# Performance work log

Hardware: AMD Instinct MI355X
Metric: run time of the kernel (lower is better)

The kernel has to match this reference:

```python
import jax, jax.numpy as jnp
import numpy as np


def _maxpool2x2(t):
    # t: [B, C, H, W] -> [B, C, H//2, W//2]
    B, C, H, W = t.shape
    return t.reshape(B, C, H // 2, 2, W // 2, 2).max(axis=(3, 5))


def setup_inputs() -> dict:
    key = jax.random.key(0)
    ks = jax.random.split(key, 6)
    ch = 64
    B, H, W = 16, 64, 64
    x = jax.random.normal(ks[0], (B, ch, H, W), dtype=jnp.float32)
    # 1x1 conv weights (spectral-norm wrapper just rescales weights; use unit-scale weights)
    w_theta = jax.random.normal(ks[1], (ch // 8, ch), dtype=jnp.float32) * 0.05
    w_phi = jax.random.normal(ks[2], (ch // 8, ch), dtype=jnp.float32) * 0.05
    w_g = jax.random.normal(ks[3], (ch // 2, ch), dtype=jnp.float32) * 0.05
    w_o = jax.random.normal(ks[4], (ch, ch // 2), dtype=jnp.float32) * 0.05
    gamma = jnp.float32(0.5)  # nonzero so attention branch contributes
    return {"x": x, "w_theta": w_theta, "w_phi": w_phi, "w_g": w_g, "w_o": w_o, "gamma": gamma}


def reference(x, w_theta, w_phi, w_g, w_o, gamma):
    B, C, H, W = x.shape
    N = H * W
    # 1x1 convs are channel contractions
    theta = jnp.einsum('oc,bchw->bohw', w_theta, x).reshape(B, -1, N)          # [B, C/8, N]
    phi = _maxpool2x2(jnp.einsum('oc,bchw->bohw', w_phi, x)).reshape(B, -1, N // 4)  # [B, C/8, N/4]
    g = _maxpool2x2(jnp.einsum('oc,bchw->bohw', w_g, x)).reshape(B, -1, N // 4)      # [B, C/2, N/4]
    # attention: no scaling (faithful to source)
    scores = jnp.einsum('bdn,bdm->bnm', theta, phi)       # [B, N, N/4]
    beta = jax.nn.softmax(scores, axis=-1)
    o = jnp.einsum('bdm,bnm->bdn', g, beta)               # [B, C/2, N]
    o = o.reshape(B, C // 2, H, W)
    o = jnp.einsum('oc,bchw->bohw', w_o, o)               # [B, C, H, W]
    return gamma * o + x
```

## Files before the change

### kernel.cpp

```cpp
#include <hip/hip_runtime.h>
#include <hip/hip_bf16.h>

#define BB 16
#define CC 64
#define NN 4096
#define MM 1024
#define LOG2E 1.4426950408889634f

typedef unsigned short u16;
typedef unsigned int u32;
typedef __attribute__((ext_vector_type(8))) short bf16x8;
typedef __attribute__((ext_vector_type(4))) float f32x4;

__device__ inline u16 f2bf(float f) {
    union { float f; u32 u; } v; v.f = f;
    return (u16)((v.u + 0x7FFFu + ((v.u >> 16) & 1u)) >> 16);
}
__device__ inline bf16x8 ld_bf16x8(const u16* p) {
    union { uint4 u; bf16x8 b; } c; c.u = *(const uint4*)p; return c.b;
}
__device__ inline bf16x8 ld2_bf16x8(const u16* p0, const u16* p1) {
    union { uint2 u[2]; bf16x8 b; } c;
    c.u[0] = *(const uint2*)p0;
    c.u[1] = *(const uint2*)p1;
    return c.b;
}
__device__ inline u32 cvt_pk_bf16(float lo, float hi) {
    __hip_bfloat162 h = __float22bfloat162_rn(make_float2(lo, hi));
    return *(u32*)&h;
}


__global__ __launch_bounds__(256) void prep_kernel(
    const float* __restrict__ x, const float* __restrict__ w_theta,
    const float* __restrict__ w_phi, const float* __restrict__ w_g,
    u16* __restrict__ theta_b, u16* __restrict__ phi_b, u16* __restrict__ gT_b)
{
    const int t = threadIdx.x, w = t >> 6, lane = t & 63;
    const int m16 = lane & 15, quad = lane >> 4;
    const int b = blockIdx.y, bx = blockIdx.x;
    const int nbase = bx * 128;

    bf16x8 A[3][2];
    {
        const float* row0 = (m16 < 8) ? (w_theta + m16 * 64) : (w_phi + (m16 - 8) * 64);
        const float* rows[3] = { row0, w_g + m16 * 64, w_g + (16 + m16) * 64 };
        #pragma unroll
        for (int f = 0; f < 3; ++f) {
            #pragma unroll
            for (int kc = 0; kc < 2; ++kc) {
                const float* p = rows[f] + kc * 32 + quad * 8;
                const float4 f0 = *(const float4*)p;
                const float4 f1 = *(const float4*)(p + 4);
                union { u32 d[4]; bf16x8 v; } a;
                a.d[0] = cvt_pk_bf16(f0.x, f0.y);
                a.d[1] = cvt_pk_bf16(f0.z, f0.w);
                a.d[2] = cvt_pk_bf16(f1.x, f1.y);
                a.d[3] = cvt_pk_bf16(f1.z, f1.w);
                A[f][kc] = a.v;
            }
        }
    }

    const float* xb = x + (size_t)b * CC * NN;
    const f32x4 zero4 = {0.f, 0.f, 0.f, 0.f};
    f32x4 acc[2][3];
    #pragma unroll
    for (int r = 0; r < 2; ++r)
        #pragma unroll
        for (int f = 0; f < 3; ++f) acc[r][f] = zero4;

    #pragma unroll
    for (int r = 0; r < 2; ++r) {
        const int px = nbase + r * 64 + w * 16 + m16;
        #pragma unroll
        for (int kc = 0; kc < 2; ++kc) {
            float xv[8];
            #pragma unroll
            for (int j = 0; j < 8; ++j)
                xv[j] = xb[(size_t)(kc * 32 + quad * 8 + j) * NN + px];
            union { u32 d[4]; bf16x8 v; } bxf;
            bxf.d[0] = cvt_pk_bf16(xv[0], xv[1]);
            bxf.d[1] = cvt_pk_bf16(xv[2], xv[3]);
            bxf.d[2] = cvt_pk_bf16(xv[4], xv[5]);
            bxf.d[3] = cvt_pk_bf16(xv[6], xv[7]);
            #pragma unroll
            for (int f = 0; f < 3; ++f)
                acc[r][f] = __builtin_amdgcn_mfma_f32_16x16x32_bf16(A[f][kc], bxf.v, acc[r][f], 0, 0, 0);
        }
    }

    if (quad < 2) {
        #pragma unroll
        for (int r = 0; r < 2; ++r) {
            const int px = nbase + r * 64 + w * 16 + m16;
            uint2 v;
            v.x = cvt_pk_bf16(acc[r][0][0] * LOG2E, acc[r][0][1] * LOG2E);
            v.y = cvt_pk_bf16(acc[r][0][2] * LOG2E, acc[r][0][3] * LOG2E);
            *(uint2*)(theta_b + ((size_t)b * NN + px) * 8 + quad * 4) = v;
        }
    }

    float pv[3][4];
    #pragma unroll
    for (int f = 0; f < 3; ++f)
        #pragma unroll
        for (int rr = 0; rr < 4; ++rr) {
            float h0 = acc[0][f][rr]; h0 = fmaxf(h0, __shfl_xor(h0, 1, 64));
            float h1 = acc[1][f][rr]; h1 = fmaxf(h1, __shfl_xor(h1, 1, 64));
            pv[f][rr] = fmaxf(h0, h1);
        }

    if ((m16 & 1) == 0) {
        const int pcol = w * 8 + (m16 >> 1);
        const int m = bx * 32 + pcol;
        if (quad >= 2) {
            uint2 v;
            v.x = cvt_pk_bf16(pv[0][0], pv[0][1]);
            v.y = cvt_pk_bf16(pv[0][2], pv[0][3]);
            *(uint2*)(phi_b + ((size_t)b * MM + m) * 8 + (quad - 2) * 4) = v;
        }
        #pragma unroll
        for (int f = 1; f < 3; ++f)
            #pragma unroll
            for (int rr = 0; rr < 4; ++rr) {
                const int d = (f - 1) * 16 + quad * 4 + rr;
                gT_b[(size_t)b * 32 * MM + (size_t)d * MM + m] = f2bf(pv[f][rr]);
            }
    }
}

__global__ __launch_bounds__(256, 2) void attn_out_kernel(
    const u16* __restrict__ theta_b, const u16* __restrict__ phi_b,
    const u16* __restrict__ gT_b, const float* __restrict__ w_o,
    const float* __restrict__ x, const float* __restrict__ gamma_p,
    float* __restrict__ out)
{
    __shared__ u16 phis[1024 * 8];
    __shared__ u16 gs[32 * 264];
    __shared__ u16 oS[128 * 40];

    const int t = threadIdx.x, w = t >> 6, lane = t & 63;
    const int m16 = lane & 15, quad = lane >> 4;
    const int b = blockIdx.y, qbase = blockIdx.x * 128;

    const u16* phg = phi_b + (size_t)b * MM * 8;
    const u16* gtg = gT_b + (size_t)b * 32 * MM;

    #pragma unroll
    for (int i = 0; i < 4; ++i)
        ((uint4*)phis)[i * 256 + t] = ((const uint4*)phg)[i * 256 + t];

    bf16x8 thB[2] = {{0,0,0,0,0,0,0,0}, {0,0,0,0,0,0,0,0}};
    if (quad == 0) {
        #pragma unroll
        for (int u = 0; u < 2; ++u)
            thB[u] = ld_bf16x8(theta_b + ((size_t)b * NN + qbase + w * 32 + u * 16 + m16) * 8);
    }

    bf16x8 woA[4];
    #pragma unroll
    for (int cf = 0; cf < 4; ++cf) {
        const float* wp = w_o + (cf * 16 + m16) * 32 + quad * 8;
        const float4 f0 = *(const float4*)wp;
        const float4 f1 = *(const float4*)(wp + 4);
        union { u32 d[4]; bf16x8 v; } a;
        a.d[0] = cvt_pk_bf16(f0.x, f0.y);
        a.d[1] = cvt_pk_bf16(f0.z, f0.w);
        a.d[2] = cvt_pk_bf16(f1.x, f1.y);
        a.d[3] = cvt_pk_bf16(f1.z, f1.w);
        woA[cf] = a.v;
    }

    bf16x8 onesA;
    #pragma unroll
    for (int i = 0; i < 8; ++i) onesA[i] = (short)0x3F80;

    const f32x4 zero4 = {0.f, 0.f, 0.f, 0.f};
    f32x4 oT0[2] = {zero4, zero4}, oT1[2] = {zero4, zero4}, lacc[2] = {zero4, zero4};

    uint4 r[4];
    #pragma unroll
    for (int i = 0; i < 4; ++i) {
        const int f = i * 256 + t, d = f >> 5, ku = f & 31;
        r[i] = *(const uint4*)(gtg + (size_t)d * MM + ku * 8);
    }

    for (int c = 0; c < 4; ++c) {
        __syncthreads();
        #pragma unroll
        for (int i = 0; i < 4; ++i) {
            const int f = i * 256 + t, d = f >> 5, ku = f & 31;
            *(uint4*)(gs + d * 264 + ku * 8) = r[i];
        }
        __syncthreads();
        if (c < 3) {
            #pragma unroll
            for (int i = 0; i < 4; ++i) {
                const int f = i * 256 + t, d = f >> 5, ku = f & 31;
                r[i] = *(const uint4*)(gtg + (size_t)d * MM + (c + 1) * 256 + ku * 8);
            }
        }

        #pragma unroll
        for (int kblk = 0; kblk < 8; ++kblk) {
            const int kb = c * 256 + kblk * 32;
            bf16x8 phA0 = {0, 0, 0, 0, 0, 0, 0, 0};
            bf16x8 phA1 = {0, 0, 0, 0, 0, 0, 0, 0};
            if (quad == 0) {
                phA0 = ld_bf16x8(phis + (size_t)(kb + m16) * 8);
                phA1 = ld_bf16x8(phis + (size_t)(kb + 16 + m16) * 8);
            }
            const u16* g0p = gs + m16 * 264 + kblk * 32 + quad * 4;
            const u16* g1p = gs + (16 + m16) * 264 + kblk * 32 + quad * 4;
            const bf16x8 gA0 = ld2_bf16x8(g0p, g0p + 16);
            const bf16x8 gA1 = ld2_bf16x8(g1p, g1p + 16);

            #pragma unroll
            for (int u = 0; u < 2; ++u) {
                const f32x4 Sa = __builtin_amdgcn_mfma_f32_16x16x32_bf16(phA0, thB[u], zero4, 0, 0, 0);
                const f32x4 Sb = __builtin_amdgcn_mfma_f32_16x16x32_bf16(phA1, thB[u], zero4, 0, 0, 0);

                union { u32 d[4]; bf16x8 v; } pb;
                pb.d[0] = cvt_pk_bf16(exp2f(Sa[0]), exp2f(Sa[1]));
                pb.d[1] = cvt_pk_bf16(exp2f(Sa[2]), exp2f(Sa[3]));
                pb.d[2] = cvt_pk_bf16(exp2f(Sb[0]), exp2f(Sb[1]));
                pb.d[3] = cvt_pk_bf16(exp2f(Sb[2]), exp2f(Sb[3]));

                oT0[u]  = __builtin_amdgcn_mfma_f32_16x16x32_bf16(gA0, pb.v, oT0[u], 0, 0, 0);
                oT1[u]  = __builtin_amdgcn_mfma_f32_16x16x32_bf16(gA1, pb.v, oT1[u], 0, 0, 0);
                lacc[u] = __builtin_amdgcn_mfma_f32_16x16x32_bf16(onesA, pb.v, lacc[u], 0, 0, 0);
            }
        }
    }

    #pragma unroll
    for (int u = 0; u < 2; ++u) {
        const float inv = 1.0f / lacc[u][0];
        u16* orow = oS + (size_t)(w * 32 + u * 16 + m16) * 40;
        uint2 a, b2;
        a.x  = cvt_pk_bf16(oT0[u][0] * inv, oT0[u][1] * inv);
        a.y  = cvt_pk_bf16(oT0[u][2] * inv, oT0[u][3] * inv);
        b2.x = cvt_pk_bf16(oT1[u][0] * inv, oT1[u][1] * inv);
        b2.y = cvt_pk_bf16(oT1[u][2] * inv, oT1[u][3] * inv);
        *(uint2*)(orow + quad * 4) = a;
        *(uint2*)(orow + 16 + quad * 4) = b2;
    }
    __syncthreads();

    const float gamma = *gamma_p;
    #pragma unroll
    for (int u = 0; u < 2; ++u) {
        const bf16x8 oB = ld_bf16x8(oS + (size_t)(w * 32 + u * 16 + m16) * 40 + quad * 8);
        #pragma unroll
        for (int cf = 0; cf < 4; ++cf) {
            const f32x4 D = __builtin_amdgcn_mfma_f32_16x16x32_bf16(woA[cf], oB, zero4, 0, 0, 0);
            #pragma unroll
            for (int rr = 0; rr < 4; ++rr) {
                const int cch = cf * 16 + quad * 4 + rr;
                const size_t adr = ((size_t)b * CC + cch) * NN + qbase + w * 32 + u * 16 + m16;
                out[adr] = gamma * D[rr] + x[adr];
            }
        }
    }
}

extern "C" void kernel_launch(void* const* d_in, const int* in_sizes, int n_in,
                              void* d_out, int out_size, void* d_ws, size_t ws_size,
                              hipStream_t stream) {
    const float* x       = (const float*)d_in[0];
    const float* w_theta = (const float*)d_in[1];
    const float* w_phi   = (const float*)d_in[2];
    const float* w_g     = (const float*)d_in[3];
    const float* w_o     = (const float*)d_in[4];
    const float* gamma   = (const float*)d_in[5];

    u16* theta_b = (u16*)d_ws;
    u16* phi_b   = theta_b + 524288;
    u16* gT_b    = phi_b + 131072;
    float* out   = (float*)d_out;

    prep_kernel<<<dim3(32, 16), 256, 0, stream>>>(x, w_theta, w_phi, w_g,
                                                  theta_b, phi_b, gT_b);
    attn_out_kernel<<<dim3(32, 16), 256, 0, stream>>>(theta_b, phi_b, gT_b,
                                                      w_o, x, gamma, out);
}
```

Baseline: 115.0 us.

## Fuse projection and attention into one kernel, recomputing phi/g per block

Merges the prep and attention kernels into a single launch, so theta, phi and g no longer go through a global workspace. Each block recomputes the pooled phi and g projections for its whole image into shared memory, in two halves, and keeps its own theta tile in LDS. The block index is swizzled so neighbouring blocks work on different batches, which is meant to improve L2 reuse of x. The cost is large redundant work: every one of the 32 blocks per image rereads all of x and redoes the 1x1 projections, in exchange for removing one launch and the workspace round trip.

```diff
diff --git a/kernel.cpp b/kernel.cpp
--- a/kernel.cpp
+++ b/kernel.cpp
@@ -30,23 +30,30 @@
     return *(u32*)&h;
 }
 
-
-__global__ __launch_bounds__(256) void prep_kernel(
+__global__ __launch_bounds__(256, 2) void fused_kernel(
     const float* __restrict__ x, const float* __restrict__ w_theta,
     const float* __restrict__ w_phi, const float* __restrict__ w_g,
-    u16* __restrict__ theta_b, u16* __restrict__ phi_b, u16* __restrict__ gT_b)
+    const float* __restrict__ w_o, const float* __restrict__ gamma_p,
+    float* __restrict__ out)
 {
+    __shared__ u16 phS[512 * 8];
+    __shared__ u16 gsS[32 * 520];
+    __shared__ u16 thS[128 * 8];
+    __shared__ u16 oS[128 * 40];
+
     const int t = threadIdx.x, w = t >> 6, lane = t & 63;
     const int m16 = lane & 15, quad = lane >> 4;
-    const int b = blockIdx.y, bx = blockIdx.x;
-    const int nbase = bx * 128;
+    const int j = blockIdx.x;
+    const int b  = (j & 7) + ((j >> 8) << 3);
+    const int qt = (j >> 3) & 31;
+    const int qbase = qt * 128;
 
     bf16x8 A[3][2];
     {
         const float* row0 = (m16 < 8) ? (w_theta + m16 * 64) : (w_phi + (m16 - 8) * 64);
         const float* rows[3] = { row0, w_g + m16 * 64, w_g + (16 + m16) * 64 };
         #pragma unroll
-        for (int f = 0; f < 3; ++f) {
+        for (int f = 0; f < 3; ++f)
             #pragma unroll
             for (int kc = 0; kc < 2; ++kc) {
                 const float* p = rows[f] + kc * 32 + quad * 8;
@@ -59,103 +66,6 @@
                 a.d[3] = cvt_pk_bf16(f1.z, f1.w);
                 A[f][kc] = a.v;
             }
-        }
-    }
-
-    const float* xb = x + (size_t)b * CC * NN;
-    const f32x4 zero4 = {0.f, 0.f, 0.f, 0.f};
-    f32x4 acc[2][3];
-    #pragma unroll
-    for (int r = 0; r < 2; ++r)
-        #pragma unroll
-        for (int f = 0; f < 3; ++f) acc[r][f] = zero4;
-
-    #pragma unroll
-    for (int r = 0; r < 2; ++r) {
-        const int px = nbase + r * 64 + w * 16 + m16;
-        #pragma unroll
-        for (int kc = 0; kc < 2; ++kc) {
-            float xv[8];
-            #pragma unroll
-            for (int j = 0; j < 8; ++j)
-                xv[j] = xb[(size_t)(kc * 32 + quad * 8 + j) * NN + px];
-            union { u32 d[4]; bf16x8 v; } bxf;
-            bxf.d[0] = cvt_pk_bf16(xv[0], xv[1]);
-            bxf.d[1] = cvt_pk_bf16(xv[2], xv[3]);
-            bxf.d[2] = cvt_pk_bf16(xv[4], xv[5]);
-            bxf.d[3] = cvt_pk_bf16(xv[6], xv[7]);
-            #pragma unroll
-            for (int f = 0; f < 3; ++f)
-                acc[r][f] = __builtin_amdgcn_mfma_f32_16x16x32_bf16(A[f][kc], bxf.v, acc[r][f], 0, 0, 0);
-        }
-    }
-
-    if (quad < 2) {
-        #pragma unroll
-        for (int r = 0; r < 2; ++r) {
-            const int px = nbase + r * 64 + w * 16 + m16;
-            uint2 v;
-            v.x = cvt_pk_bf16(acc[r][0][0] * LOG2E, acc[r][0][1] * LOG2E);
-            v.y = cvt_pk_bf16(acc[r][0][2] * LOG2E, acc[r][0][3] * LOG2E);
-            *(uint2*)(theta_b + ((size_t)b * NN + px) * 8 + quad * 4) = v;
-        }
-    }
-
-    float pv[3][4];
-    #pragma unroll
-    for (int f = 0; f < 3; ++f)
-        #pragma unroll
-        for (int rr = 0; rr < 4; ++rr) {
-            float h0 = acc[0][f][rr]; h0 = fmaxf(h0, __shfl_xor(h0, 1, 64));
-            float h1 = acc[1][f][rr]; h1 = fmaxf(h1, __shfl_xor(h1, 1, 64));
-            pv[f][rr] = fmaxf(h0, h1);
-        }
-
-    if ((m16 & 1) == 0) {
-        const int pcol = w * 8 + (m16 >> 1);
-        const int m = bx * 32 + pcol;
-        if (quad >= 2) {
-            uint2 v;
-            v.x = cvt_pk_bf16(pv[0][0], pv[0][1]);
-            v.y = cvt_pk_bf16(pv[0][2], pv[0][3]);
-            *(uint2*)(phi_b + ((size_t)b * MM + m) * 8 + (quad - 2) * 4) = v;
-        }
-        #pragma unroll
-        for (int f = 1; f < 3; ++f)
-            #pragma unroll
-            for (int rr = 0; rr < 4; ++rr) {
-                const int d = (f - 1) * 16 + quad * 4 + rr;
-                gT_b[(size_t)b * 32 * MM + (size_t)d * MM + m] = f2bf(pv[f][rr]);
-            }
-    }
-}
-
-__global__ __launch_bounds__(256, 2) void attn_out_kernel(
-    const u16* __restrict__ theta_b, const u16* __restrict__ phi_b,
-    const u16* __restrict__ gT_b, const float* __restrict__ w_o,
-    const float* __restrict__ x, const float* __restrict__ gamma_p,
-    float* __restrict__ out)
-{
-    __shared__ u16 phis[1024 * 8];
-    __shared__ u16 gs[32 * 264];
-    __shared__ u16 oS[128 * 40];
-
-    const int t = threadIdx.x, w = t >> 6, lane = t & 63;
-    const int m16 = lane & 15, quad = lane >> 4;
-    const int b = blockIdx.y, qbase = blockIdx.x * 128;
-
-    const u16* phg = phi_b + (size_t)b * MM * 8;
-    const u16* gtg = gT_b + (size_t)b * 32 * MM;
-
-    #pragma unroll
-    for (int i = 0; i < 4; ++i)
-        ((uint4*)phis)[i * 256 + t] = ((const uint4*)phg)[i * 256 + t];
-
-    bf16x8 thB[2] = {{0,0,0,0,0,0,0,0}, {0,0,0,0,0,0,0,0}};
-    if (quad == 0) {
-        #pragma unroll
-        for (int u = 0; u < 2; ++u)
-            thB[u] = ld_bf16x8(theta_b + ((size_t)b * NN + qbase + w * 32 + u * 16 + m16) * 8);
     }
 
     bf16x8 woA[4];
@@ -171,48 +81,100 @@
         a.d[3] = cvt_pk_bf16(f1.z, f1.w);
         woA[cf] = a.v;
     }
-
     bf16x8 onesA;
     #pragma unroll
     for (int i = 0; i < 8; ++i) onesA[i] = (short)0x3F80;
 
+    const float* xb = x + (size_t)b * CC * NN;
     const f32x4 zero4 = {0.f, 0.f, 0.f, 0.f};
     f32x4 oT0[2] = {zero4, zero4}, oT1[2] = {zero4, zero4}, lacc[2] = {zero4, zero4};
-
-    uint4 r[4];
-    #pragma unroll
-    for (int i = 0; i < 4; ++i) {
-        const int f = i * 256 + t, d = f >> 5, ku = f & 31;
-        r[i] = *(const uint4*)(gtg + (size_t)d * MM + ku * 8);
-    }
-
-    for (int c = 0; c < 4; ++c) {
+    bf16x8 thB[2] = {{0,0,0,0,0,0,0,0}, {0,0,0,0,0,0,0,0}};
+
+    const int c0 = qt >> 4;
+
+    for (int cc = 0; cc < 2; ++cc) {
+        const int c = (cc == 0) ? c0 : 1 - c0;
+
+        for (int i = 0; i < 4; ++i) {
+            const int pr = c * 16 + w * 4 + i;
+            for (int cg = 0; cg < 4; ++cg) {
+                f32x4 f0r[2], f1r[2], f2r[2];
+                #pragma unroll
+                for (int r = 0; r < 2; ++r) {
+                    const int px = (2 * pr + r) * 64 + cg * 16 + m16;
+                    f32x4 a0 = zero4, a1 = zero4, a2 = zero4;
+                    #pragma unroll
+                    for (int kc = 0; kc < 2; ++kc) {
+                        float xv[8];
+                        #pragma unroll
+                        for (int jj = 0; jj < 8; ++jj)
+                            xv[jj] = xb[(size_t)(kc * 32 + quad * 8 + jj) * NN + px];
+                        union { u32 d[4]; bf16x8 v; } bxf;
+                        bxf.d[0] = cvt_pk_bf16(xv[0], xv[1]);
+                        bxf.d[1] = cvt_pk_bf16(xv[2], xv[3]);
+                        bxf.d[2] = cvt_pk_bf16(xv[4], xv[5]);
+                        bxf.d[3] = cvt_pk_bf16(xv[6], xv[7]);
+                        a0 = __builtin_amdgcn_mfma_f32_16x16x32_bf16(A[0][kc], bxf.v, a0, 0, 0, 0);
+                        a1 = __builtin_amdgcn_mfma_f32_16x16x32_bf16(A[1][kc], bxf.v, a1, 0, 0, 0);
+                        a2 = __builtin_amdgcn_mfma_f32_16x16x32_bf16(A[2][kc], bxf.v, a2, 0, 0, 0);
+                    }
+                    f0r[r] = a0; f1r[r] = a1; f2r[r] = a2;
+                    if (pr == qt && quad < 2) {
+                        const int ql = r * 64 + cg * 16 + m16;
+                        uint2 v;
+                        v.x = cvt_pk_bf16(a0[0] * LOG2E, a0[1] * LOG2E);
+                        v.y = cvt_pk_bf16(a0[2] * LOG2E, a0[3] * LOG2E);
+                        *(uint2*)(thS + ql * 8 + quad * 4) = v;
+                    }
+                }
+                float pv0[4], pv1[4], pv2[4];
+                #pragma unroll
+                for (int rr = 0; rr < 4; ++rr) {
+                    float h0, h1;
+                    h0 = f0r[0][rr]; h0 = fmaxf(h0, __shfl_xor(h0, 1, 64));
+                    h1 = f0r[1][rr]; h1 = fmaxf(h1, __shfl_xor(h1, 1, 64));
+                    pv0[rr] = fmaxf(h0, h1);
+                    h0 = f1r[0][rr]; h0 = fmaxf(h0, __shfl_xor(h0, 1, 64));
+                    h1 = f1r[1][rr]; h1 = fmaxf(h1, __shfl_xor(h1, 1, 64));
+                    pv1[rr] = fmaxf(h0, h1);
+                    h0 = f2r[0][rr]; h0 = fmaxf(h0, __shfl_xor(h0, 1, 64));
+                    h1 = f2r[1][rr]; h1 = fmaxf(h1, __shfl_xor(h1, 1, 64));
+                    pv2[rr] = fmaxf(h0, h1);
+                }
+                if ((m16 & 1) == 0) {
+                    const int ml = (pr - c * 16) * 32 + cg * 8 + (m16 >> 1);
+                    if (quad >= 2) {
+                        uint2 v;
+                        v.x = cvt_pk_bf16(pv0[0], pv0[1]);
+                        v.y = cvt_pk_bf16(pv0[2], pv0[3]);
+                        *(uint2*)(phS + ml * 8 + (quad - 2) * 4) = v;
+                    }
+                    #pragma unroll
+                    for (int rr = 0; rr < 4; ++rr) {
+                        gsS[(quad * 4 + rr) * 520 + ml]        = f2bf(pv1[rr]);
+                        gsS[(16 + quad * 4 + rr) * 520 + ml]   = f2bf(pv2[rr]);
+                    }
+                }
+            }
+        }
         __syncthreads();
-        #pragma unroll
-        for (int i = 0; i < 4; ++i) {
-            const int f = i * 256 + t, d = f >> 5, ku = f & 31;
-            *(uint4*)(gs + d * 264 + ku * 8) = r[i];
-        }
-        __syncthreads();
-        if (c < 3) {
-            #pragma unroll
-            for (int i = 0; i < 4; ++i) {
-                const int f = i * 256 + t, d = f >> 5, ku = f & 31;
-                r[i] = *(const uint4*)(gtg + (size_t)d * MM + (c + 1) * 256 + ku * 8);
-            }
-        }
-
-        #pragma unroll
-        for (int kblk = 0; kblk < 8; ++kblk) {
-            const int kb = c * 256 + kblk * 32;
+
+        if (cc == 0 && quad == 0) {
+            thB[0] = ld_bf16x8(thS + (w * 32 + m16) * 8);
+            thB[1] = ld_bf16x8(thS + (w * 32 + 16 + m16) * 8);
+        }
+
+        #pragma unroll 4
+        for (int kblk = 0; kblk < 16; ++kblk) {
+            const int kb = kblk * 32;
             bf16x8 phA0 = {0, 0, 0, 0, 0, 0, 0, 0};
             bf16x8 phA1 = {0, 0, 0, 0, 0, 0, 0, 0};
             if (quad == 0) {
-                phA0 = ld_bf16x8(phis + (size_t)(kb + m16) * 8);
-                phA1 = ld_bf16x8(phis + (size_t)(kb + 16 + m16) * 8);
-            }
-            const u16* g0p = gs + m16 * 264 + kblk * 32 + quad * 4;
-            const u16* g1p = gs + (16 + m16) * 264 + kblk * 32 + quad * 4;
+                phA0 = ld_bf16x8(phS + (kb + m16) * 8);
+                phA1 = ld_bf16x8(phS + (kb + 16 + m16) * 8);
+            }
+            const u16* g0p = gsS + m16 * 520 + kb + quad * 4;
+            const u16* g1p = gsS + (16 + m16) * 520 + kb + quad * 4;
             const bf16x8 gA0 = ld2_bf16x8(g0p, g0p + 16);
             const bf16x8 gA1 = ld2_bf16x8(g1p, g1p + 16);
 
@@ -220,18 +182,17 @@
             for (int u = 0; u < 2; ++u) {
                 const f32x4 Sa = __builtin_amdgcn_mfma_f32_16x16x32_bf16(phA0, thB[u], zero4, 0, 0, 0);
                 const f32x4 Sb = __builtin_amdgcn_mfma_f32_16x16x32_bf16(phA1, thB[u], zero4, 0, 0, 0);
-
                 union { u32 d[4]; bf16x8 v; } pb;
                 pb.d[0] = cvt_pk_bf16(exp2f(Sa[0]), exp2f(Sa[1]));
                 pb.d[1] = cvt_pk_bf16(exp2f(Sa[2]), exp2f(Sa[3]));
                 pb.d[2] = cvt_pk_bf16(exp2f(Sb[0]), exp2f(Sb[1]));
                 pb.d[3] = cvt_pk_bf16(exp2f(Sb[2]), exp2f(Sb[3]));
-
                 oT0[u]  = __builtin_amdgcn_mfma_f32_16x16x32_bf16(gA0, pb.v, oT0[u], 0, 0, 0);
                 oT1[u]  = __builtin_amdgcn_mfma_f32_16x16x32_bf16(gA1, pb.v, oT1[u], 0, 0, 0);
                 lacc[u] = __builtin_amdgcn_mfma_f32_16x16x32_bf16(onesA, pb.v, lacc[u], 0, 0, 0);
             }
         }
+        __syncthreads();
     }
 
     #pragma unroll
@@ -246,8 +207,6 @@
         *(uint2*)(orow + quad * 4) = a;
         *(uint2*)(orow + 16 + quad * 4) = b2;
     }
-    __syncthreads();
-
     const float gamma = *gamma_p;
     #pragma unroll
     for (int u = 0; u < 2; ++u) {
@@ -274,14 +233,8 @@
     const float* w_g     = (const float*)d_in[3];
     const float* w_o     = (const float*)d_in[4];
     const float* gamma   = (const float*)d_in[5];
-
-    u16* theta_b = (u16*)d_ws;
-    u16* phi_b   = theta_b + 524288;
-    u16* gT_b    = phi_b + 131072;
-    float* out   = (float*)d_out;
-
-    prep_kernel<<<dim3(32, 16), 256, 0, stream>>>(x, w_theta, w_phi, w_g,
-                                                  theta_b, phi_b, gT_b);
-    attn_out_kernel<<<dim3(32, 16), 256, 0, stream>>>(theta_b, phi_b, gT_b,
-                                                      w_o, x, gamma, out);
-}
+    float* out = (float*)d_out;
+
+    fused_kernel<<<dim3(512), 256, 0, stream>>>(x, w_theta, w_phi, w_g,
+                                                w_o, gamma, out);
+}
```

New measurement: 145.3 us. +26.4%, slower.
